# Performance work log

Measured on AMD Instinct MI355X. Metric: run time of the kernel, lower is better.

The kernel has to match this reference:

```python
import jax, jax.numpy as jnp
import numpy as np

ALPHA = 1.702
LIMIT = 7.0

E, H, D = 16, 1024, 1024  # num_experts, hidden_size, expert_dim
B, S = 1, 2048


def setup_inputs() -> dict:
    key = jax.random.key(0)
    ks = jax.random.split(key, 6)
    return {
        "hidden_states": jax.random.normal(ks[0], (B, S, H), dtype=jnp.float32),
        "routing_weights": jax.random.uniform(ks[1], (B * S, E), dtype=jnp.float32),
        "gate_up_proj": jax.random.normal(ks[2], (E, H, 2 * D), dtype=jnp.float32) * 0.02,
        "gate_up_proj_bias": jax.random.normal(ks[3], (E, 2 * D), dtype=jnp.float32) * 0.02,
        "down_proj": jax.random.normal(ks[4], (E, D, H), dtype=jnp.float32) * 0.02,
        "down_proj_bias": jax.random.normal(ks[5], (E, H), dtype=jnp.float32) * 0.02,
    }


def reference(hidden_states, routing_weights, gate_up_proj, gate_up_proj_bias,
              down_proj, down_proj_bias):
    batch = hidden_states.shape[0]
    hs = hidden_states.reshape(-1, H)  # [T, H], T = B*S
    # dense per-expert gate_up projection: [E, T, 2D]
    gate_up = jnp.einsum('th,ehd->etd', hs, gate_up_proj) + gate_up_proj_bias[:, None, :]
    gate = gate_up[..., ::2]   # [E, T, D]
    up = gate_up[..., 1::2]    # [E, T, D]
    gate = jnp.minimum(gate, LIMIT)
    up = jnp.clip(up, -LIMIT, LIMIT)
    glu = gate * jax.nn.sigmoid(gate * ALPHA)
    # down projection: [E, T, H]
    next_states = jnp.einsum('etd,edh->eth', (up + 1.0) * glu, down_proj)
    next_states = next_states + down_proj_bias[:, None, :]
    # weighted sum over experts with routing_weights [T, E]
    out = jnp.einsum('eth,te->th', next_states, routing_weights)
    return out.reshape(batch, -1, H)
```

## Files before the change

### kernel.cpp

```cpp
#include <hip/hip_runtime.h>
#include <hip/hip_bf16.h>
#include <cstdint>
#include <cstddef>

#define E_     16
#define H_     1024
#define D_     1024
#define T_     2048
#define TWO_D  2048
#define KFLAT  (E_ * D_)

typedef float  f32x4  __attribute__((ext_vector_type(4)));
typedef short  bf16x8 __attribute__((ext_vector_type(8)));

static __device__ __forceinline__ unsigned short f2bf(float f) {
  union { float f; unsigned u; } v; v.f = f;
  unsigned u = v.u;
  unsigned r = (u + 0x7FFFu + ((u >> 16) & 1u)) >> 16;
  return (unsigned short)r;
}

static __device__ __forceinline__ void gload16(const void* g, void* l) {
  __builtin_amdgcn_global_load_lds(
      (const __attribute__((address_space(1))) void*)g,
      (__attribute__((address_space(3))) void*)l, 16, 0, 0);
}

__global__ void k_trans_gu(const float* __restrict__ gu,
                           unsigned short* __restrict__ wg,
                           unsigned short* __restrict__ wu) {
  __shared__ float tile[64][65];
  const int e  = blockIdx.z;
  const int h0 = blockIdx.y * 64;
  const int c0 = blockIdx.x * 64;
  const int tid = threadIdx.x;
  const float* src = gu + (size_t)e * H_ * TWO_D;
#pragma unroll
  for (int i = 0; i < 16; ++i) {
    int lin = tid + i * 256;
    int hr = lin >> 6, c = lin & 63;
    tile[hr][c] = src[(size_t)(h0 + hr) * TWO_D + c0 + c];
  }
  __syncthreads();
  const int d0 = c0 >> 1;
#pragma unroll
  for (int i = 0; i < 4; ++i) {
    int lin = tid + i * 256;
    int dg = lin >> 5, hp = lin & 31;
    int h = hp * 2;
    ushort2 o = make_ushort2(f2bf(tile[h][dg * 2]), f2bf(tile[h + 1][dg * 2]));
    *(ushort2*)&wg[(((size_t)e << 10) + d0 + dg) * H_ + h0 + h] = o;
  }
#pragma unroll
  for (int i = 0; i < 4; ++i) {
    int lin = tid + i * 256;
    int dg = lin >> 5, hp = lin & 31;
    int h = hp * 2;
    ushort2 o = make_ushort2(f2bf(tile[h][dg * 2 + 1]), f2bf(tile[h + 1][dg * 2 + 1]));
    *(ushort2*)&wu[(((size_t)e << 10) + d0 + dg) * H_ + h0 + h] = o;
  }
}

__global__ void k_trans_dn(const float* __restrict__ dn,
                           unsigned short* __restrict__ wd) {
  __shared__ float tile[64][65];
  const int e  = blockIdx.z;
  const int d0 = blockIdx.y * 64;
  const int h0 = blockIdx.x * 64;
  const int tid = threadIdx.x;
  const float* src = dn + (size_t)e * D_ * H_;
#pragma unroll
  for (int i = 0; i < 16; ++i) {
    int lin = tid + i * 256;
    int dr = lin >> 6, hc = lin & 63;
    tile[dr][hc] = src[(size_t)(d0 + dr) * H_ + h0 + hc];
  }
  __syncthreads();
#pragma unroll
  for (int i = 0; i < 8; ++i) {
    int lin = tid + i * 256;
    int hr = lin >> 5, dp = lin & 31;
    ushort2 o = make_ushort2(f2bf(tile[dp * 2][hr]), f2bf(tile[dp * 2 + 1][hr]));
    *(ushort2*)&wd[(size_t)(h0 + hr) * KFLAT + (e << 10) + d0 + dp * 2] = o;
  }
}

__global__ void k_cvt_hs(const float* __restrict__ hs, unsigned short* __restrict__ hb) {
  int idx = blockIdx.x * blockDim.x + threadIdx.x;
  float4 v = ((const float4*)hs)[idx];
  ushort4 o;
  o.x = f2bf(v.x); o.y = f2bf(v.y); o.z = f2bf(v.z); o.w = f2bf(v.w);
  ((ushort4*)hb)[idx] = o;
}

__global__ void k_bias_out(const float* __restrict__ rw, const float* __restrict__ db,
                           float* __restrict__ out) {
  int idx = blockIdx.x * blockDim.x + threadIdx.x;
  int t = idx >> 10, h = idx & 1023;
  const float* r = rw + t * E_;
  float acc = 0.f;
#pragma unroll
  for (int e = 0; e < E_; ++e) acc += r[e] * db[(e << 10) + h];
  out[idx] = acc;
}

__global__ void __launch_bounds__(512, 2)
k_gemm1(const unsigned short* __restrict__ hb,
        const unsigned short* __restrict__ wg,
        const unsigned short* __restrict__ wu,
        const float* __restrict__ gub,
        const float* __restrict__ rw,
        unsigned short* __restrict__ act) {
  __shared__ __align__(16) short lsA[2][256 * 64];
  __shared__ __align__(16) short lsB[2][256 * 64];
  const int e     = blockIdx.z;
  const int t0    = blockIdx.y * 256;
  const int d0blk = blockIdx.x * 128;
  const int tid  = threadIdx.x;
  const int lane = tid & 63;
  const int w    = tid >> 6;
  const int wm = w >> 2, wn = w & 3;
  const int lo = lane & 15, hi = lane >> 4;

  const unsigned short* aS[4];
  const unsigned short* bS[4];
  int ldst[4];
#pragma unroll
  for (int i = 0; i < 4; ++i) {
    int lin = tid + i * 512;
    int row = lin >> 3, ch = lin & 7;
    int sch = ch ^ (row & 7);
    ldst[i] = lin * 8;
    aS[i] = hb + (size_t)(t0 + row) * H_ + sch * 8;
    int dl = ((row >> 5) << 4) + (row & 15);
    const unsigned short* bp = ((row >> 4) & 1) ? wu : wg;
    bS[i] = bp + (((size_t)e << 10) + d0blk + dl) * H_ + sch * 8;
  }

#define G1_STAGE(buf, k0)                                                      \
  {                                                                            \
    _Pragma("unroll")                                                          \
    for (int i = 0; i < 4; ++i) gload16(aS[i] + (k0), &lsA[buf][ldst[i]]);     \
    _Pragma("unroll")                                                          \
    for (int i = 0; i < 4; ++i) gload16(bS[i] + (k0), &lsB[buf][ldst[i]]);     \
  }

  f32x4 acc[8][4];
#pragma unroll
  for (int mi = 0; mi < 8; ++mi)
#pragma unroll
    for (int nf = 0; nf < 4; ++nf) acc[mi][nf] = (f32x4)0.f;

  const int cb0 = ((0 | hi) ^ (lo & 7)) << 3;
  const int cb1 = ((4 | hi) ^ (lo & 7)) << 3;
  const int arow = (wm * 128 + lo) * 64;
  const int brow = (wn * 64 + lo) * 64;

#define G1_COMPUTE(cur)                                                        \
  {                                                                            \
    bf16x8 bfr[4], af[4];                                                      \
                                                   \
    _Pragma("unroll")                                                          \
    for (int nf = 0; nf < 4; ++nf) bfr[nf] = *(const bf16x8*)&lsB[cur][brow + nf * 1024 + cb0]; \
    _Pragma("unroll")                                                          \
    for (int mi = 0; mi < 4; ++mi) af[mi] = *(const bf16x8*)&lsA[cur][arow + mi * 1024 + cb0];  \
    __builtin_amdgcn_s_setprio(1);                                             \
    _Pragma("unroll")                                                          \
    for (int mi = 0; mi < 4; ++mi)                                             \
      _Pragma("unroll")                                                        \
      for (int nf = 0; nf < 4; ++nf)                                           \
        acc[mi][nf] = __builtin_amdgcn_mfma_f32_16x16x32_bf16(af[mi], bfr[nf], acc[mi][nf], 0, 0, 0); \
    __builtin_amdgcn_s_setprio(0);                                             \
                                                   \
    _Pragma("unroll")                                                          \
    for (int mi = 0; mi < 4; ++mi) af[mi] = *(const bf16x8*)&lsA[cur][arow + (mi + 4) * 1024 + cb0]; \
    __builtin_amdgcn_s_setprio(1);                                             \
    _Pragma("unroll")                                                          \
    for (int mi = 0; mi < 4; ++mi)                                             \
      _Pragma("unroll")                                                        \
      for (int nf = 0; nf < 4; ++nf)                                           \
        acc[mi + 4][nf] = __builtin_amdgcn_mfma_f32_16x16x32_bf16(af[mi], bfr[nf], acc[mi + 4][nf], 0, 0, 0); \
    __builtin_amdgcn_s_setprio(0);                                             \
                                                   \
    _Pragma("unroll")                                                          \
    for (int nf = 0; nf < 4; ++nf) bfr[nf] = *(const bf16x8*)&lsB[cur][brow + nf * 1024 + cb1]; \
    _Pragma("unroll")                                                          \
    for (int mi = 0; mi < 4; ++mi) af[mi] = *(const bf16x8*)&lsA[cur][arow + mi * 1024 + cb1];  \
    __builtin_amdgcn_s_setprio(1);                                             \
    _Pragma("unroll")                                                          \
    for (int mi = 0; mi < 4; ++mi)                                             \
      _Pragma("unroll")                                                        \
      for (int nf = 0; nf < 4; ++nf)                                           \
        acc[mi][nf] = __builtin_amdgcn_mfma_f32_16x16x32_bf16(af[mi], bfr[nf], acc[mi][nf], 0, 0, 0); \
    __builtin_amdgcn_s_setprio(0);                                             \
                                                   \
    _Pragma("unroll")                                                          \
    for (int mi = 0; mi < 4; ++mi) af[mi] = *(const bf16x8*)&lsA[cur][arow + (mi + 4) * 1024 + cb1]; \
    __builtin_amdgcn_s_setprio(1);                                             \
    _Pragma("unroll")                                                          \
    for (int mi = 0; mi < 4; ++mi)                                             \
      _Pragma("unroll")                                                        \
      for (int nf = 0; nf < 4; ++nf)                                           \
        acc[mi + 4][nf] = __builtin_amdgcn_mfma_f32_16x16x32_bf16(af[mi], bfr[nf], acc[mi + 4][nf], 0, 0, 0); \
    __builtin_amdgcn_s_setprio(0);                                             \
  }

  G1_STAGE(0, 0);
  for (int kt = 0; kt < 15; ++kt) {
    const int cur = kt & 1;
    G1_STAGE(cur ^ 1, (kt + 1) * 64);
    asm volatile("s_waitcnt vmcnt(8)\n\ts_barrier" ::: "memory");
    G1_COMPUTE(cur);
    asm volatile("s_barrier" ::: "memory");
  }
  asm volatile("s_waitcnt vmcnt(0)\n\ts_barrier" ::: "memory");
  G1_COMPUTE(1);
#undef G1_STAGE
#undef G1_COMPUTE

  float gb[2], ub[2];
#pragma unroll
  for (int j = 0; j < 2; ++j) {
    const int d = d0blk + (wn * 2 + j) * 16 + lo;
    gb[j] = gub[e * TWO_D + 2 * d];
    ub[j] = gub[e * TWO_D + 2 * d + 1];
  }
#pragma unroll
  for (int mi = 0; mi < 8; ++mi) {
#pragma unroll
    for (int rr = 0; rr < 4; ++rr) {
      const int t = t0 + wm * 128 + mi * 16 + hi * 4 + rr;
      const float r = rw[t * E_ + e];
#pragma unroll
      for (int j = 0; j < 2; ++j) {
        const int d = d0blk + (wn * 2 + j) * 16 + lo;
        float g = acc[mi][2 * j][rr]     + gb[j];
        float u = acc[mi][2 * j + 1][rr] + ub[j];
        g = fminf(g, 7.0f);
        u = fminf(fmaxf(u, -7.0f), 7.0f);
        float glu = g / (1.0f + __expf(-1.702f * g));
        act[(size_t)t * KFLAT + (e << 10) + d] = f2bf((u + 1.0f) * glu * r);
      }
    }
  }
}

__global__ void __launch_bounds__(256)
k_gemm2(const unsigned short* __restrict__ act,
        const unsigned short* __restrict__ wd,
        float* __restrict__ out) {
  __shared__ __align__(16) short lsA[2][128 * 64];
  __shared__ __align__(16) short lsB[2][128 * 64];
  const int ks_blk = blockIdx.z;
  const int t0 = blockIdx.y * 128;
  const int h0 = blockIdx.x * 128;
  const int tid  = threadIdx.x;
  const int lane = tid & 63;
  const int w    = tid >> 6;
  const int wm = w >> 1, wn = w & 1;
  const int lo = lane & 15, hi = lane >> 4;

  f32x4 acc[4][4];
#pragma unroll
  for (int mi = 0; mi < 4; ++mi)
#pragma unroll
    for (int nf = 0; nf < 4; ++nf) acc[mi][nf] = (f32x4)0.f;

#define G2_STAGE(buf, k0)                                                      \
  {                                                                            \
    _Pragma("unroll")                                                          \
    for (int i = 0; i < 4; ++i) {                                              \
      int lin = tid + i * 256; int row = lin >> 3, ch = lin & 7;               \
      int sch = ch ^ (row & 7);                                                \
      gload16(act + (size_t)(t0 + row) * KFLAT + (k0) + sch * 8,               \
              &lsA[buf][lin * 8]);                                             \
    }                                                                          \
    _Pragma("unroll")                                                          \
    for (int i = 0; i < 4; ++i) {                                              \
      int lin = tid + i * 256; int row = lin >> 3, ch = lin & 7;               \
      int sch = ch ^ (row & 7);                                                \
      gload16(wd + (size_t)(h0 + row) * KFLAT + (k0) + sch * 8,                \
              &lsB[buf][lin * 8]);                                             \
    }                                                                          \
  }

  const int kbeg = ks_blk * (KFLAT / 4);
  const int NKT  = (KFLAT / 4) / 64;
  G2_STAGE(0, kbeg);
  __syncthreads();
  int cur = 0;
  for (int kt = 0; kt < NKT; ++kt) {
    if (kt + 1 < NKT) G2_STAGE(cur ^ 1, kbeg + (kt + 1) * 64);
#pragma unroll
    for (int ks = 0; ks < 2; ++ks) {
      const int cb = (((ks << 2) | hi) ^ (lo & 7)) << 3;
      bf16x8 af[4], bfr[4];
#pragma unroll
      for (int mi = 0; mi < 4; ++mi)
        af[mi] = *(const bf16x8*)&lsA[cur][(wm * 64 + mi * 16 + lo) * 64 + cb];
#pragma unroll
      for (int nf = 0; nf < 4; ++nf)
        bfr[nf] = *(const bf16x8*)&lsB[cur][(wn * 64 + nf * 16 + lo) * 64 + cb];
#pragma unroll
      for (int mi = 0; mi < 4; ++mi)
#pragma unroll
        for (int nf = 0; nf < 4; ++nf)
          acc[mi][nf] = __builtin_amdgcn_mfma_f32_16x16x32_bf16(af[mi], bfr[nf], acc[mi][nf], 0, 0, 0);
    }
    __syncthreads();
    cur ^= 1;
  }
#undef G2_STAGE

#pragma unroll
  for (int mi = 0; mi < 4; ++mi) {
#pragma unroll
    for (int rr = 0; rr < 4; ++rr) {
      const int t = t0 + wm * 64 + mi * 16 + hi * 4 + rr;
#pragma unroll
      for (int nf = 0; nf < 4; ++nf) {
        const int h = h0 + wn * 64 + nf * 16 + lo;
        atomicAdd(&out[(size_t)t * H_ + h], acc[mi][nf][rr]);
      }
    }
  }
}

extern "C" void kernel_launch(void* const* d_in, const int* in_sizes, int n_in,
                              void* d_out, int out_size, void* d_ws, size_t ws_size,
                              hipStream_t stream) {
  const float* hs  = (const float*)d_in[0];
  const float* rw  = (const float*)d_in[1];
  const float* gup = (const float*)d_in[2];
  const float* gub = (const float*)d_in[3];
  const float* dnp = (const float*)d_in[4];
  const float* dnb = (const float*)d_in[5];
  float* out = (float*)d_out;

  char* ws = (char*)d_ws;
  unsigned short* hb  = (unsigned short*)(ws);
  unsigned short* wg  = (unsigned short*)(ws + (4UL   << 20));
  unsigned short* wu  = (unsigned short*)(ws + (36UL  << 20));
  unsigned short* wd  = (unsigned short*)(ws + (68UL  << 20));
  unsigned short* act = (unsigned short*)(ws + (100UL << 20));

  k_cvt_hs  <<<(T_ * H_ / 4) / 256, 256, 0, stream>>>(hs, hb);
  k_trans_gu<<<dim3(TWO_D / 64, H_ / 64, E_), 256, 0, stream>>>(gup, wg, wu);
  k_trans_dn<<<dim3(H_ / 64, D_ / 64, E_),    256, 0, stream>>>(dnp, wd);
  k_bias_out<<<(T_ * H_) / 256, 256, 0, stream>>>(rw, dnb, out);
  k_gemm1   <<<dim3(TWO_D / 256, T_ / 256, E_), 512, 0, stream>>>(hb, wg, wu, gub, rw, act);
  k_gemm2   <<<dim3(H_ / 128, T_ / 128, 4),   256, 0, stream>>>(act, wd, out);
}
```

Measured before the change: 531.5 us.

## Retile down-projection GEMM to 256x256 blocks and vectorize weight transposes

The second GEMM moves from 128x128 tiles with 4 warps and a 4-way K split to 256x256 tiles with 8 warps and an 8-way K split. It reuses the first GEMM's software-pipelined compute macro with vmcnt-based waits and precomputed load pointers. The weight transpose kernels now read with float4 loads and write ushort4 bf16 outputs over larger tiles. The aim is more data reuse per block and fewer, wider memory transactions, at the cost of more shared memory, more registers, and more atomic traffic from the deeper K split.

```diff
diff --git a/kernel.cpp b/kernel.cpp
--- a/kernel.cpp
+++ b/kernel.cpp
@@ -29,59 +29,63 @@
 __global__ void k_trans_gu(const float* __restrict__ gu,
                            unsigned short* __restrict__ wg,
                            unsigned short* __restrict__ wu) {
-  __shared__ float tile[64][65];
+  __shared__ float tile[64][130];
   const int e  = blockIdx.z;
   const int h0 = blockIdx.y * 64;
-  const int c0 = blockIdx.x * 64;
+  const int c0 = blockIdx.x * 128;
   const int tid = threadIdx.x;
   const float* src = gu + (size_t)e * H_ * TWO_D;
 #pragma unroll
-  for (int i = 0; i < 16; ++i) {
-    int lin = tid + i * 256;
-    int hr = lin >> 6, c = lin & 63;
-    tile[hr][c] = src[(size_t)(h0 + hr) * TWO_D + c0 + c];
+  for (int i = 0; i < 8; ++i) {
+    int item = tid + i * 256;
+    int row = item >> 5, fc = item & 31;
+    float4 v = *(const float4*)&src[(size_t)(h0 + row) * TWO_D + c0 + fc * 4];
+    *(float2*)&tile[row][fc * 4]     = make_float2(v.x, v.y);
+    *(float2*)&tile[row][fc * 4 + 2] = make_float2(v.z, v.w);
   }
   __syncthreads();
   const int d0 = c0 >> 1;
 #pragma unroll
   for (int i = 0; i < 4; ++i) {
-    int lin = tid + i * 256;
-    int dg = lin >> 5, hp = lin & 31;
-    int h = hp * 2;
-    ushort2 o = make_ushort2(f2bf(tile[h][dg * 2]), f2bf(tile[h + 1][dg * 2]));
-    *(ushort2*)&wg[(((size_t)e << 10) + d0 + dg) * H_ + h0 + h] = o;
-  }
-#pragma unroll
-  for (int i = 0; i < 4; ++i) {
-    int lin = tid + i * 256;
-    int dg = lin >> 5, hp = lin & 31;
-    int h = hp * 2;
-    ushort2 o = make_ushort2(f2bf(tile[h][dg * 2 + 1]), f2bf(tile[h + 1][dg * 2 + 1]));
-    *(ushort2*)&wu[(((size_t)e << 10) + d0 + dg) * H_ + h0 + h] = o;
+    int item = tid + i * 256;
+    int dg = item >> 4, hq = item & 15;
+    const int c = dg * 2;
+    ushort4 og, ou;
+    og.x = f2bf(tile[hq * 4 + 0][c]);     og.y = f2bf(tile[hq * 4 + 1][c]);
+    og.z = f2bf(tile[hq * 4 + 2][c]);     og.w = f2bf(tile[hq * 4 + 3][c]);
+    ou.x = f2bf(tile[hq * 4 + 0][c + 1]); ou.y = f2bf(tile[hq * 4 + 1][c + 1]);
+    ou.z = f2bf(tile[hq * 4 + 2][c + 1]); ou.w = f2bf(tile[hq * 4 + 3][c + 1]);
+    const size_t o = (((size_t)e << 10) + d0 + dg) * H_ + h0 + hq * 4;
+    *(ushort4*)&wg[o] = og;
+    *(ushort4*)&wu[o] = ou;
   }
 }
 
 __global__ void k_trans_dn(const float* __restrict__ dn,
                            unsigned short* __restrict__ wd) {
-  __shared__ float tile[64][65];
+  __shared__ float tile[128][66];
   const int e  = blockIdx.z;
-  const int d0 = blockIdx.y * 64;
+  const int d0 = blockIdx.y * 128;
   const int h0 = blockIdx.x * 64;
   const int tid = threadIdx.x;
   const float* src = dn + (size_t)e * D_ * H_;
 #pragma unroll
-  for (int i = 0; i < 16; ++i) {
-    int lin = tid + i * 256;
-    int dr = lin >> 6, hc = lin & 63;
-    tile[dr][hc] = src[(size_t)(d0 + dr) * H_ + h0 + hc];
+  for (int i = 0; i < 8; ++i) {
+    int item = tid + i * 256;
+    int row = item >> 4, fc = item & 15;
+    float4 v = *(const float4*)&src[(size_t)(d0 + row) * H_ + h0 + fc * 4];
+    *(float2*)&tile[row][fc * 4]     = make_float2(v.x, v.y);
+    *(float2*)&tile[row][fc * 4 + 2] = make_float2(v.z, v.w);
   }
   __syncthreads();
 #pragma unroll
   for (int i = 0; i < 8; ++i) {
-    int lin = tid + i * 256;
-    int hr = lin >> 5, dp = lin & 31;
-    ushort2 o = make_ushort2(f2bf(tile[dp * 2][hr]), f2bf(tile[dp * 2 + 1][hr]));
-    *(ushort2*)&wd[(size_t)(h0 + hr) * KFLAT + (e << 10) + d0 + dp * 2] = o;
+    int item = tid + i * 256;
+    int hr = item >> 5, dq = item & 31;
+    ushort4 o;
+    o.x = f2bf(tile[dq * 4 + 0][hr]); o.y = f2bf(tile[dq * 4 + 1][hr]);
+    o.z = f2bf(tile[dq * 4 + 2][hr]); o.w = f2bf(tile[dq * 4 + 3][hr]);
+    *(ushort4*)&wd[(size_t)(h0 + hr) * KFLAT + (e << 10) + d0 + dq * 4] = o;
   }
 }
 
@@ -156,14 +160,13 @@
   const int arow = (wm * 128 + lo) * 64;
   const int brow = (wn * 64 + lo) * 64;
 
-#define G1_COMPUTE(cur)                                                        \
+#define G_COMPUTE(LA, LB)                                                      \
   {                                                                            \
     bf16x8 bfr[4], af[4];                                                      \
-                                                   \
-    _Pragma("unroll")                                                          \
-    for (int nf = 0; nf < 4; ++nf) bfr[nf] = *(const bf16x8*)&lsB[cur][brow + nf * 1024 + cb0]; \
-    _Pragma("unroll")                                                          \
-    for (int mi = 0; mi < 4; ++mi) af[mi] = *(const bf16x8*)&lsA[cur][arow + mi * 1024 + cb0];  \
+    _Pragma("unroll")                                                          \
+    for (int nf = 0; nf < 4; ++nf) bfr[nf] = *(const bf16x8*)&LB[brow + nf * 1024 + cb0]; \
+    _Pragma("unroll")                                                          \
+    for (int mi = 0; mi < 4; ++mi) af[mi] = *(const bf16x8*)&LA[arow + mi * 1024 + cb0];  \
     __builtin_amdgcn_s_setprio(1);                                             \
     _Pragma("unroll")                                                          \
     for (int mi = 0; mi < 4; ++mi)                                             \
@@ -171,9 +174,8 @@
       for (int nf = 0; nf < 4; ++nf)                                           \
         acc[mi][nf] = __builtin_amdgcn_mfma_f32_16x16x32_bf16(af[mi], bfr[nf], acc[mi][nf], 0, 0, 0); \
     __builtin_amdgcn_s_setprio(0);                                             \
-                                                   \
-    _Pragma("unroll")                                                          \
-    for (int mi = 0; mi < 4; ++mi) af[mi] = *(const bf16x8*)&lsA[cur][arow + (mi + 4) * 1024 + cb0]; \
+    _Pragma("unroll")                                                          \
+    for (int mi = 0; mi < 4; ++mi) af[mi] = *(const bf16x8*)&LA[arow + (mi + 4) * 1024 + cb0]; \
     __builtin_amdgcn_s_setprio(1);                                             \
     _Pragma("unroll")                                                          \
     for (int mi = 0; mi < 4; ++mi)                                             \
@@ -181,11 +183,10 @@
       for (int nf = 0; nf < 4; ++nf)                                           \
         acc[mi + 4][nf] = __builtin_amdgcn_mfma_f32_16x16x32_bf16(af[mi], bfr[nf], acc[mi + 4][nf], 0, 0, 0); \
     __builtin_amdgcn_s_setprio(0);                                             \
-                                                   \
-    _Pragma("unroll")                                                          \
-    for (int nf = 0; nf < 4; ++nf) bfr[nf] = *(const bf16x8*)&lsB[cur][brow + nf * 1024 + cb1]; \
-    _Pragma("unroll")                                                          \
-    for (int mi = 0; mi < 4; ++mi) af[mi] = *(const bf16x8*)&lsA[cur][arow + mi * 1024 + cb1];  \
+    _Pragma("unroll")                                                          \
+    for (int nf = 0; nf < 4; ++nf) bfr[nf] = *(const bf16x8*)&LB[brow + nf * 1024 + cb1]; \
+    _Pragma("unroll")                                                          \
+    for (int mi = 0; mi < 4; ++mi) af[mi] = *(const bf16x8*)&LA[arow + mi * 1024 + cb1];  \
     __builtin_amdgcn_s_setprio(1);                                             \
     _Pragma("unroll")                                                          \
     for (int mi = 0; mi < 4; ++mi)                                             \
@@ -193,9 +194,8 @@
       for (int nf = 0; nf < 4; ++nf)                                           \
         acc[mi][nf] = __builtin_amdgcn_mfma_f32_16x16x32_bf16(af[mi], bfr[nf], acc[mi][nf], 0, 0, 0); \
     __builtin_amdgcn_s_setprio(0);                                             \
-                                                   \
-    _Pragma("unroll")                                                          \
-    for (int mi = 0; mi < 4; ++mi) af[mi] = *(const bf16x8*)&lsA[cur][arow + (mi + 4) * 1024 + cb1]; \
+    _Pragma("unroll")                                                          \
+    for (int mi = 0; mi < 4; ++mi) af[mi] = *(const bf16x8*)&LA[arow + (mi + 4) * 1024 + cb1]; \
     __builtin_amdgcn_s_setprio(1);                                             \
     _Pragma("unroll")                                                          \
     for (int mi = 0; mi < 4; ++mi)                                             \
@@ -210,13 +210,12 @@
     const int cur = kt & 1;
     G1_STAGE(cur ^ 1, (kt + 1) * 64);
     asm volatile("s_waitcnt vmcnt(8)\n\ts_barrier" ::: "memory");
-    G1_COMPUTE(cur);
+    if (cur == 0) G_COMPUTE(lsA[0], lsB[0]) else G_COMPUTE(lsA[1], lsB[1]);
     asm volatile("s_barrier" ::: "memory");
   }
   asm volatile("s_waitcnt vmcnt(0)\n\ts_barrier" ::: "memory");
-  G1_COMPUTE(1);
+  G_COMPUTE(lsA[1], lsB[1]);
 #undef G1_STAGE
-#undef G1_COMPUTE
 
   float gb[2], ub[2];
 #pragma unroll
@@ -245,78 +244,70 @@
   }
 }
 
-__global__ void __launch_bounds__(256)
+__global__ void __launch_bounds__(512, 2)
 k_gemm2(const unsigned short* __restrict__ act,
         const unsigned short* __restrict__ wd,
         float* __restrict__ out) {
-  __shared__ __align__(16) short lsA[2][128 * 64];
-  __shared__ __align__(16) short lsB[2][128 * 64];
-  const int ks_blk = blockIdx.z;
-  const int t0 = blockIdx.y * 128;
-  const int h0 = blockIdx.x * 128;
+  __shared__ __align__(16) short lsA[2][256 * 64];
+  __shared__ __align__(16) short lsB[2][256 * 64];
+  const int t0   = blockIdx.y * 256;
+  const int h0   = blockIdx.x * 256;
+  const int kbeg = blockIdx.z * (KFLAT / 8);
   const int tid  = threadIdx.x;
   const int lane = tid & 63;
   const int w    = tid >> 6;
-  const int wm = w >> 1, wn = w & 1;
+  const int wm = w >> 2, wn = w & 3;
   const int lo = lane & 15, hi = lane >> 4;
 
-  f32x4 acc[4][4];
-#pragma unroll
-  for (int mi = 0; mi < 4; ++mi)
-#pragma unroll
-    for (int nf = 0; nf < 4; ++nf) acc[mi][nf] = (f32x4)0.f;
+  const unsigned short* aS[4];
+  const unsigned short* bS[4];
+  int ldst[4];
+#pragma unroll
+  for (int i = 0; i < 4; ++i) {
+    int lin = tid + i * 512;
+    int row = lin >> 3, ch = lin & 7;
+    int sch = ch ^ (row & 7);
+    ldst[i] = lin * 8;
+    aS[i] = act + (size_t)(t0 + row) * KFLAT + kbeg + sch * 8;
+    bS[i] = wd  + (size_t)(h0 + row) * KFLAT + kbeg + sch * 8;
+  }
 
 #define G2_STAGE(buf, k0)                                                      \
   {                                                                            \
     _Pragma("unroll")                                                          \
-    for (int i = 0; i < 4; ++i) {                                              \
-      int lin = tid + i * 256; int row = lin >> 3, ch = lin & 7;               \
-      int sch = ch ^ (row & 7);                                                \
-      gload16(act + (size_t)(t0 + row) * KFLAT + (k0) + sch * 8,               \
-              &lsA[buf][lin * 8]);                                             \
-    }                                                                          \
-    _Pragma("unroll")                                                          \
-    for (int i = 0; i < 4; ++i) {                                              \
-      int lin = tid + i * 256; int row = lin >> 3, ch = lin & 7;               \
-      int sch = ch ^ (row & 7);                                                \
-      gload16(wd + (size_t)(h0 + row) * KFLAT + (k0) + sch * 8,                \
-              &lsB[buf][lin * 8]);                                             \
-    }                                                                          \
-  }
-
-  const int kbeg = ks_blk * (KFLAT / 4);
-  const int NKT  = (KFLAT / 4) / 64;
-  G2_STAGE(0, kbeg);
-  __syncthreads();
-  int cur = 0;
-  for (int kt = 0; kt < NKT; ++kt) {
-    if (kt + 1 < NKT) G2_STAGE(cur ^ 1, kbeg + (kt + 1) * 64);
-#pragma unroll
-    for (int ks = 0; ks < 2; ++ks) {
-      const int cb = (((ks << 2) | hi) ^ (lo & 7)) << 3;
-      bf16x8 af[4], bfr[4];
-#pragma unroll
-      for (int mi = 0; mi < 4; ++mi)
-        af[mi] = *(const bf16x8*)&lsA[cur][(wm * 64 + mi * 16 + lo) * 64 + cb];
-#pragma unroll
-      for (int nf = 0; nf < 4; ++nf)
-        bfr[nf] = *(const bf16x8*)&lsB[cur][(wn * 64 + nf * 16 + lo) * 64 + cb];
-#pragma unroll
-      for (int mi = 0; mi < 4; ++mi)
-#pragma unroll
-        for (int nf = 0; nf < 4; ++nf)
-          acc[mi][nf] = __builtin_amdgcn_mfma_f32_16x16x32_bf16(af[mi], bfr[nf], acc[mi][nf], 0, 0, 0);
-    }
-    __syncthreads();
-    cur ^= 1;
-  }
+    for (int i = 0; i < 4; ++i) gload16(aS[i] + (k0), &lsA[buf][ldst[i]]);     \
+    _Pragma("unroll")                                                          \
+    for (int i = 0; i < 4; ++i) gload16(bS[i] + (k0), &lsB[buf][ldst[i]]);     \
+  }
+
+  f32x4 acc[8][4];
+#pragma unroll
+  for (int mi = 0; mi < 8; ++mi)
+#pragma unroll
+    for (int nf = 0; nf < 4; ++nf) acc[mi][nf] = (f32x4)0.f;
+
+  const int cb0 = ((0 | hi) ^ (lo & 7)) << 3;
+  const int cb1 = ((4 | hi) ^ (lo & 7)) << 3;
+  const int arow = (wm * 128 + lo) * 64;
+  const int brow = (wn * 64 + lo) * 64;
+
+  G2_STAGE(0, 0);
+  for (int kt = 0; kt < 31; ++kt) {
+    const int cur = kt & 1;
+    G2_STAGE(cur ^ 1, (kt + 1) * 64);
+    asm volatile("s_waitcnt vmcnt(8)\n\ts_barrier" ::: "memory");
+    if (cur == 0) G_COMPUTE(lsA[0], lsB[0]) else G_COMPUTE(lsA[1], lsB[1]);
+    asm volatile("s_barrier" ::: "memory");
+  }
+  asm volatile("s_waitcnt vmcnt(0)\n\ts_barrier" ::: "memory");
+  G_COMPUTE(lsA[1], lsB[1]);
 #undef G2_STAGE
 
 #pragma unroll
-  for (int mi = 0; mi < 4; ++mi) {
+  for (int mi = 0; mi < 8; ++mi) {
 #pragma unroll
     for (int rr = 0; rr < 4; ++rr) {
-      const int t = t0 + wm * 64 + mi * 16 + hi * 4 + rr;
+      const int t = t0 + wm * 128 + mi * 16 + hi * 4 + rr;
 #pragma unroll
       for (int nf = 0; nf < 4; ++nf) {
         const int h = h0 + wn * 64 + nf * 16 + lo;
@@ -345,9 +336,9 @@
   unsigned short* act = (unsigned short*)(ws + (100UL << 20));
 
   k_cvt_hs  <<<(T_ * H_ / 4) / 256, 256, 0, stream>>>(hs, hb);
-  k_trans_gu<<<dim3(TWO_D / 64, H_ / 64, E_), 256, 0, stream>>>(gup, wg, wu);
-  k_trans_dn<<<dim3(H_ / 64, D_ / 64, E_),    256, 0, stream>>>(dnp, wd);
+  k_trans_gu<<<dim3(TWO_D / 128, H_ / 64, E_), 256, 0, stream>>>(gup, wg, wu);
+  k_trans_dn<<<dim3(H_ / 64, D_ / 128, E_),    256, 0, stream>>>(dnp, wd);
   k_bias_out<<<(T_ * H_) / 256, 256, 0, stream>>>(rw, dnb, out);
   k_gemm1   <<<dim3(TWO_D / 256, T_ / 256, E_), 512, 0, stream>>>(hb, wg, wu, gub, rw, act);
-  k_gemm2   <<<dim3(H_ / 128, T_ / 128, 4),   256, 0, stream>>>(act, wd, out);
-}
+  k_gemm2   <<<dim3(H_ / 256, T_ / 256, 8),     512, 0, stream>>>(act, wd, out);
+}
```

Result: slower. 1.610 ms (+202.9%).
